# Kernel tuning notes

Measured on AMD Instinct MI355X. Metric: run time of the kernel, lower is better.

Reference implementation:

```python
import jax, jax.numpy as jnp
import numpy as np

N_NODES = 100000
N_EDGES = 1600000
NFEAT = 128
NHID = 128
NCLASS = 40


def gcn_conv(x, W, b, src, dst, n_nodes):
    """PyG-style GCNConv: x' = D^{-1/2}(A+I)D^{-1/2} (x W) + b."""
    h = x @ W  # [N, out]
    loop = jnp.arange(n_nodes, dtype=src.dtype)
    s = jnp.concatenate([src, loop])  # add self-loops
    d = jnp.concatenate([dst, loop])
    deg = jax.ops.segment_sum(jnp.ones_like(s, dtype=h.dtype), d, num_segments=n_nodes)
    dinv = jnp.where(deg > 0, jax.lax.rsqrt(deg), 0.0)
    norm = dinv[s] * dinv[d]  # [E+N]
    msg = h[s] * norm[:, None]  # gather + scale
    out = jax.ops.segment_sum(msg, d, num_segments=n_nodes)  # scatter-add
    return out + b


def setup_inputs() -> dict:
    key = jax.random.key(0)
    ks = jax.random.split(key, 6)
    x = jax.random.normal(ks[0], (N_NODES, NFEAT), dtype=jnp.float32)
    edge_index = jax.random.randint(ks[1], (2, N_EDGES), 0, N_NODES, dtype=jnp.int64)
    sc1 = 1.0 / np.sqrt(NFEAT)
    sc2 = 1.0 / np.sqrt(NHID)
    W1 = jax.random.normal(ks[2], (NFEAT, NHID), dtype=jnp.float32) * sc1
    b1 = jnp.zeros((NHID,), dtype=jnp.float32)
    Wm = jax.random.normal(ks[3], (NHID, NHID), dtype=jnp.float32) * sc2
    bm = jnp.zeros((NHID,), dtype=jnp.float32)
    W2 = jax.random.normal(ks[4], (NHID, NCLASS), dtype=jnp.float32) * sc2
    b2 = jnp.zeros((NCLASS,), dtype=jnp.float32)
    return {"x": x, "edge_index": edge_index, "W1": W1, "b1": b1,
            "Wm": Wm, "bm": bm, "W2": W2, "b2": b2}


def reference(x, edge_index, W1, b1, Wm, bm, W2, b2):
    # StandGCNX forward, eval mode (dropout = identity)
    src, dst = edge_index[0], edge_index[1]
    n = x.shape[0]
    h = jax.nn.relu(gcn_conv(x, W1, b1, src, dst, n))
    h = jax.nn.relu(gcn_conv(h, Wm, bm, src, dst, n))
    out = gcn_conv(h, W2, b2, src, dst, n)
    return out
```

## Files before the change

kernel.cpp:

```cpp
#include <hip/hip_runtime.h>
#include <hip/hip_bf16.h>

typedef __attribute__((ext_vector_type(8))) short bf16x8;
typedef __attribute__((ext_vector_type(4))) float f32x4;

__device__ __forceinline__ ushort bf16rne(float f) {
    uint u = __float_as_uint(f);
    return (ushort)((u + 0x7fffu + ((u >> 16) & 1u)) >> 16);
}
__device__ __forceinline__ void unpack2(uint p, float& a, float& b) {
    a = __uint_as_float(p << 16);
    b = __uint_as_float(p & 0xffff0000u);
}


__global__ __launch_bounds__(256) void k_pre1(const float* __restrict__ W1,
                                              const float* __restrict__ Wm,
                                              const float* __restrict__ W2,
                                              ushort* __restrict__ w1t,
                                              ushort* __restrict__ wmt,
                                              ushort* __restrict__ w2t,
                                              const int* __restrict__ dst,
                                              int* __restrict__ bcnt, int E) {
    __shared__ int hist[512];
    int b = blockIdx.x;
    int t = threadIdx.x;
    if (b < 152) {
        if (b < 64) {
            int i = b * 256 + t; int k = i >> 7, n = i & 127;
            w1t[n * 128 + k] = bf16rne(W1[k * 128 + n]);
        } else if (b < 128) {
            int i = (b - 64) * 256 + t; int k = i >> 7, n = i & 127;
            wmt[n * 128 + k] = bf16rne(Wm[k * 128 + n]);
        } else {
            int i = (b - 128) * 256 + t;
            if (i < 6144) {
                int n = i >> 7, k = i & 127;
                w2t[n * 128 + k] = (n < 40) ? bf16rne(W2[k * 40 + n]) : (ushort)0;
            }
        }
        return;
    }
    hist[t] = 0; hist[t + 256] = 0;
    __syncthreads();
    int off = (b - 152) * 4096;
    int cnt = min(4096, E - off);
    for (int i = t; i < cnt; i += 256) atomicAdd(&hist[dst[off + i] >> 8], 1);
    __syncthreads();
    if (hist[t]) atomicAdd(&bcnt[t], hist[t]);
    if (hist[t + 256]) atomicAdd(&bcnt[t + 256], hist[t + 256]);
}

__global__ void k_bscan(const int* __restrict__ bcnt, int* __restrict__ bbase,
                        int* __restrict__ bcur, int nbuck) {
    __shared__ int s[512];
    int t = threadIdx.x;
    s[t] = (t < nbuck) ? bcnt[t] : 0;
    __syncthreads();
    for (int d = 1; d < 512; d <<= 1) {
        int u = (t >= d) ? s[t - d] : 0;
        __syncthreads();
        if (t >= d) s[t] += u;
        __syncthreads();
    }
    int excl = (t == 0) ? 0 : s[t - 1];
    bbase[t] = excl;
    if (t < nbuck) bcur[t] = excl;
    if (t == 511) bbase[512] = s[511];
}


__global__ __launch_bounds__(256) void k_pack_gemm(const int* __restrict__ src,
                                                   const int* __restrict__ dst,
                                                   int* __restrict__ bcur,
                                                   uint* __restrict__ pairbuf,
                                                   int E, int nbuck, int ntile,
                                                   const float* __restrict__ A,
                                                   const ushort* __restrict__ Wt,
                                                   ushort* __restrict__ C, int M) {
    __shared__ int hist[512];
    __shared__ int scn[512];
    __shared__ int cur[512];
    __shared__ int gbase[512];
    __shared__ uint sorted[4096];
    int t = threadIdx.x;
    if ((int)blockIdx.x >= ntile) {
        int blk = blockIdx.x - ntile;
        int wave = t >> 6, lane = t & 63;
        int m16 = lane & 15, quad = lane >> 4;
        int rowA = blk * 64 + wave * 16 + m16;
        int rA = min(rowA, M - 1);
        const float4* A4 = (const float4*)A;

        f32x4 acc[8];
#pragma unroll
        for (int i = 0; i < 8; i++) acc[i] = (f32x4){0.f, 0.f, 0.f, 0.f};
#pragma unroll
        for (int it = 0; it < 4; it++) {
            float4 f0 = A4[(size_t)rA * 32 + 8 * it + 2 * quad];
            float4 f1 = A4[(size_t)rA * 32 + 8 * it + 2 * quad + 1];
            bf16x8 af;
            af[0] = (short)bf16rne(f0.x); af[1] = (short)bf16rne(f0.y);
            af[2] = (short)bf16rne(f0.z); af[3] = (short)bf16rne(f0.w);
            af[4] = (short)bf16rne(f1.x); af[5] = (short)bf16rne(f1.y);
            af[6] = (short)bf16rne(f1.z); af[7] = (short)bf16rne(f1.w);
#pragma unroll
            for (int nt = 0; nt < 8; nt++) {
                bf16x8 bfr = *(const bf16x8*)(Wt + (size_t)(nt * 16 + m16) * 128 + it * 32 + quad * 8);
                acc[nt] = __builtin_amdgcn_mfma_f32_16x16x32_bf16(af, bfr, acc[nt], 0, 0, 0);
            }
        }
        int rowBase = blk * 64 + wave * 16 + quad * 4;
#pragma unroll
        for (int nt = 0; nt < 8; nt++) {
            int col = nt * 16 + m16;
#pragma unroll
            for (int r = 0; r < 4; r++) {
                int row = rowBase + r;
                if (row < M) C[(size_t)row * 128 + col] = bf16rne(acc[nt][r]);
            }
        }
        return;
    }
    int off = blockIdx.x * 4096;
    int cnt = min(4096, E - off);
    hist[t] = 0; hist[t + 256] = 0;
    __syncthreads();
    for (int i = t; i < cnt; i += 256) {
        int b = dst[off + i] >> 8;
        atomicAdd(&hist[b], 1);
    }
    __syncthreads();
    scn[t] = hist[t]; scn[t + 256] = hist[t + 256];
    __syncthreads();
    for (int d = 1; d < 256; d <<= 1) {
        int u0 = (t >= d) ? scn[t - d] : 0;
        int u1 = (t >= d) ? scn[256 + t - d] : 0;
        __syncthreads();
        if (t >= d) { scn[t] += u0; scn[256 + t] += u1; }
        __syncthreads();
    }
    int tot0 = scn[255];
    scn[256 + t] += tot0;
    __syncthreads();
    cur[t] = (t == 0) ? 0 : scn[t - 1];
    cur[t + 256] = scn[t + 255];
    if (t < nbuck && hist[t] > 0) gbase[t] = atomicAdd(&bcur[t], hist[t]);
    int t2 = t + 256;
    if (t2 < nbuck && hist[t2] > 0) gbase[t2] = atomicAdd(&bcur[t2], hist[t2]);
    __syncthreads();
    for (int i = t; i < cnt; i += 256) {
        int d = dst[off + i];
        int s = src[off + i];
        int b = d >> 8;
        int pos = atomicAdd(&cur[b], 1);
        sorted[pos] = ((uint)(d & 255) << 24) | (uint)s;
    }
    __syncthreads();
    int wid = t >> 6, lane = t & 63;
    for (int b = wid; b < nbuck; b += 4) {
        int n = hist[b];
        if (n == 0) continue;
        int ls = (b == 0) ? 0 : scn[b - 1];
        int gb = gbase[b];
        for (int j = lane; j < n; j += 64)
            pairbuf[gb + j] = sorted[ls + j];
    }
}

#define CSR_CAP 5632
__global__ __launch_bounds__(256) void k_csrbuild(const uint* __restrict__ pairbuf,
                                                  const int* __restrict__ bbase,
                                                  int* __restrict__ rowptr,
                                                  float* __restrict__ dinv,
                                                  int* __restrict__ csr,
                                                  int N, int nbuck) {
    __shared__ int lhist[256];
    __shared__ int scn[256];
    __shared__ int lcur[256];
    __shared__ int lcsr[CSR_CAP];
    int b = blockIdx.x;
    int base = b << 8;
    int nn = min(256, N - base);
    int lo = bbase[b], hi = bbase[b + 1];
    int cnt = hi - lo;
    int t = threadIdx.x;
    lhist[t] = 0;
    __syncthreads();
    for (int i = t; i < cnt; i += 256) atomicAdd(&lhist[pairbuf[lo + i] >> 24], 1);
    __syncthreads();
    int mydeg = lhist[t];
    scn[t] = mydeg;
    __syncthreads();
    for (int d = 1; d < 256; d <<= 1) {
        int u = (t >= d) ? scn[t - d] : 0;
        __syncthreads();
        if (t >= d) scn[t] += u;
        __syncthreads();
    }
    int excl = (t == 0) ? 0 : scn[t - 1];
    lcur[t] = excl;
    if (t < nn) {
        rowptr[base + t] = lo + excl;
        dinv[base + t] = rsqrtf((float)(mydeg + 1));
    }
    if (b == nbuck - 1 && t == 0) rowptr[N] = hi;
    __syncthreads();
    if (cnt <= CSR_CAP) {
        for (int i = t; i < cnt; i += 256) {
            uint p = pairbuf[lo + i];
            int pos = atomicAdd(&lcur[p >> 24], 1);
            lcsr[pos] = (int)(p & 0xFFFFFFu);
        }
        __syncthreads();
        for (int i = t; i < cnt; i += 256) csr[lo + i] = lcsr[i];
    } else {
        for (int i = t; i < cnt; i += 256) {
            uint p = pairbuf[lo + i];
            int pos = lo + atomicAdd(&lcur[p >> 24], 1);
            csr[pos] = (int)(p & 0xFFFFFFu);
        }
    }
}


template <bool EDGE_W>
__device__ __forceinline__ void batch8(const uint* __restrict__ g32, int lane,
                                       int creg, int wreg, int j, int lim,
                                       float& x0, float& x1) {
    uint P[8]; float W[8];
#pragma unroll
    for (int k = 0; k < 8; k++) {
        int idx = j + k;
        int cl = idx < 63 ? idx : 63;
        int s = __builtin_amdgcn_readlane(creg, cl);
        float w = EDGE_W ? __int_as_float(__builtin_amdgcn_readlane(wreg, cl)) : 1.0f;
        W[k] = (idx < lim) ? w : 0.0f;
        P[k] = g32[(size_t)s * 64 + lane];
    }
#pragma unroll
    for (int k = 0; k < 8; k++) {
        float u, v; unpack2(P[k], u, v);
        x0 += u * W[k]; x1 += v * W[k];
    }
}

template <bool EDGE_W>
__device__ __forceinline__ void batch8x2(const uint* __restrict__ g32, int lane,
                                         int cA, int wA, int jA, int limA,
                                         float& a0, float& a1,
                                         int cB, int wB, int jB, int limB,
                                         float& b0, float& b1) {
    uint PA[8], PB[8]; float WA[8], WB[8];
#pragma unroll
    for (int k = 0; k < 8; k++) {
        int idx = jA + k;
        int cl = idx < 63 ? idx : 63;
        int s = __builtin_amdgcn_readlane(cA, cl);
        float w = EDGE_W ? __int_as_float(__builtin_amdgcn_readlane(wA, cl)) : 1.0f;
        WA[k] = (idx < limA) ? w : 0.0f;
        PA[k] = g32[(size_t)s * 64 + lane];
    }
#pragma unroll
    for (int k = 0; k < 8; k++) {
        int idx = jB + k;
        int cl = idx < 63 ? idx : 63;
        int s = __builtin_amdgcn_readlane(cB, cl);
        float w = EDGE_W ? __int_as_float(__builtin_amdgcn_readlane(wB, cl)) : 1.0f;
        WB[k] = (idx < limB) ? w : 0.0f;
        PB[k] = g32[(size_t)s * 64 + lane];
    }
#pragma unroll
    for (int k = 0; k < 8; k++) {
        float u, v; unpack2(PA[k], u, v);
        a0 += u * WA[k]; a1 += v * WA[k];
    }
#pragma unroll
    for (int k = 0; k < 8; k++) {
        float u, v; unpack2(PB[k], u, v);
        b0 += u * WB[k]; b1 += v * WB[k];
    }
}

template <bool EDGE_W>
__device__ __forceinline__ void agg_node_chunked(const uint* __restrict__ g32,
                                                 const int* __restrict__ csr,
                                                 const float* __restrict__ dinv,
                                                 int lane, int e0, int e1,
                                                 float& x0, float& x1) {
    for (int base = e0; base < e1; base += 64) {
        int nc = e1 - base; if (nc > 64) nc = 64;
        int sidx = 0, swi = 0;
        if (lane < nc) {
            sidx = csr[base + lane];
            if (EDGE_W) swi = __float_as_int(dinv[sidx]);
        }
        int nc8 = (nc + 7) & ~7;
        for (int j = 0; j < nc8; j += 8)
            batch8<EDGE_W>(g32, lane, sidx, swi, j, nc, x0, x1);
    }
}

template <int NT, bool EDGE_W>
__device__ __forceinline__ void fused_agg_gemm(const ushort* __restrict__ g,
                                               const float* __restrict__ dinv,
                                               const int* __restrict__ rowptr,
                                               const int* __restrict__ csr,
                                               const float* __restrict__ bias,
                                               const ushort* __restrict__ Wt,
                                               ushort* __restrict__ C,
                                               int M, int ccols) {
    __shared__ ushort hs[32][136];
    int t = threadIdx.x;
    int lane = t & 63;
    int wave = t >> 6;
    const uint* g32 = (const uint*)g;
    float2 bb = ((const float2*)bias)[lane];

    int nodeBase = blockIdx.x * 32 + wave * 8;
    int nd_l = min(nodeBase + lane, M - 1);

    uint srow[8];
#pragma unroll
    for (int i = 0; i < 8; i++) {
        int nd = __builtin_amdgcn_readlane(nd_l, i);
        srow[i] = g32[(size_t)nd * 64 + lane];
    }
    int e0_l = 0, e1_l = 0; float dn_l = 0.f;
    if (lane < 8) {
        e0_l = rowptr[nd_l];
        e1_l = rowptr[nd_l + 1];
        dn_l = dinv[nd_l];
    }
    int c0 = 0, c1 = 0, c2 = 0, c3 = 0;
    int w0 = 0, w1 = 0, w2 = 0, w3 = 0;
    int sp0, sp1, sp2, sp3, Ls0, Ls1, Ls2, Ls3;
    sp0 = __builtin_amdgcn_readlane(e0_l, 0);
    Ls0 = __builtin_amdgcn_readlane(e1_l, 1) - sp0;
    sp1 = __builtin_amdgcn_readlane(e0_l, 2);
    Ls1 = __builtin_amdgcn_readlane(e1_l, 3) - sp1;
    sp2 = __builtin_amdgcn_readlane(e0_l, 4);
    Ls2 = __builtin_amdgcn_readlane(e1_l, 5) - sp2;
    sp3 = __builtin_amdgcn_readlane(e0_l, 6);
    Ls3 = __builtin_amdgcn_readlane(e1_l, 7) - sp3;
    if (Ls0 <= 64 && lane < Ls0) c0 = csr[sp0 + lane];
    if (Ls1 <= 64 && lane < Ls1) c1 = csr[sp1 + lane];
    if (Ls2 <= 64 && lane < Ls2) c2 = csr[sp2 + lane];
    if (Ls3 <= 64 && lane < Ls3) c3 = csr[sp3 + lane];
    if (EDGE_W) {
        if (Ls0 <= 64 && lane < Ls0) w0 = __float_as_int(dinv[c0]);
        if (Ls1 <= 64 && lane < Ls1) w1 = __float_as_int(dinv[c1]);
        if (Ls2 <= 64 && lane < Ls2) w2 = __float_as_int(dinv[c2]);
        if (Ls3 <= 64 && lane < Ls3) w3 = __float_as_int(dinv[c3]);
    }
    int cp[4] = {c0, c1, c2, c3};
    int wp[4] = {w0, w1, w2, w3};
    int spp[4] = {sp0, sp1, sp2, sp3};
    int Lsp[4] = {Ls0, Ls1, Ls2, Ls3};

#pragma unroll
    for (int p = 0; p < 4; p++) {
        int iA = 2 * p, iB = 2 * p + 1;
        int eA0 = __builtin_amdgcn_readlane(e0_l, iA);
        int eA1 = __builtin_amdgcn_readlane(e1_l, iA);
        int eB0 = __builtin_amdgcn_readlane(e0_l, iB);
        int eB1 = __builtin_amdgcn_readlane(e1_l, iB);
        float dnA = __int_as_float(__builtin_amdgcn_readlane(__float_as_int(dn_l), iA));
        float dnB = __int_as_float(__builtin_amdgcn_readlane(__float_as_int(dn_l), iB));
        float a0, a1, b0, b1;
        {
            float u, v;
            unpack2(srow[2 * p], u, v);
            if (EDGE_W) { a0 = u * dnA; a1 = v * dnA; } else { a0 = u; a1 = v; }
            unpack2(srow[2 * p + 1], u, v);
            if (EDGE_W) { b0 = u * dnB; b1 = v * dnB; } else { b0 = u; b1 = v; }
        }
        if (Lsp[p] <= 64) {
            int offA = eA0 - spp[p];
            int offB = eB0 - spp[p];
            int nA = eA1 - eA0, nB = eB1 - eB0;
            int limA = offA + nA, limB = offB + nB;
            int jA = offA, jB = offB;
            int jAend = offA + ((nA + 7) & ~7);
            int jBend = offB + ((nB + 7) & ~7);
            while (jA < jAend && jB < jBend) {
                batch8x2<EDGE_W>(g32, lane, cp[p], wp[p], jA, limA, a0, a1,
                                 cp[p], wp[p], jB, limB, b0, b1);
                jA += 8; jB += 8;
            }
            while (jA < jAend) { batch8<EDGE_W>(g32, lane, cp[p], wp[p], jA, limA, a0, a1); jA += 8; }
            while (jB < jBend) { batch8<EDGE_W>(g32, lane, cp[p], wp[p], jB, limB, b0, b1); jB += 8; }
        } else {
            agg_node_chunked<EDGE_W>(g32, csr, dinv, lane, eA0, eA1, a0, a1);
            agg_node_chunked<EDGE_W>(g32, csr, dinv, lane, eB0, eB1, b0, b1);
        }
        float o0 = fmaxf(a0 * dnA + bb.x, 0.f);
        float o1 = fmaxf(a1 * dnA + bb.y, 0.f);
        float o2 = fmaxf(b0 * dnB + bb.x, 0.f);
        float o3 = fmaxf(b1 * dnB + bb.y, 0.f);
        uint qA = (uint)bf16rne(o0) | ((uint)bf16rne(o1) << 16);
        uint qB = (uint)bf16rne(o2) | ((uint)bf16rne(o3) << 16);
        *(uint*)&hs[wave * 8 + 2 * p][lane * 2] = qA;
        *(uint*)&hs[wave * 8 + 2 * p + 1][lane * 2] = qB;
    }
    __syncthreads();

    int wv = t >> 6, lane6 = t & 63;
    int m16 = lane6 & 15, quad = lane6 >> 4;
    int rowHalf = wv & 1;
    int ntHalf = wv >> 1;
    constexpr int NTH = (NT + 1) / 2;
    int ntStart = ntHalf * NTH;
    int ntEnd = ntHalf ? NT : NTH;

    f32x4 acc[NTH];
#pragma unroll
    for (int i = 0; i < NTH; i++) acc[i] = (f32x4){0.f, 0.f, 0.f, 0.f};
#pragma unroll
    for (int it = 0; it < 4; it++) {
        bf16x8 af = *(const bf16x8*)&hs[rowHalf * 16 + m16][it * 32 + quad * 8];
        for (int nt = ntStart; nt < ntEnd; nt++) {
            bf16x8 bfr = *(const bf16x8*)(Wt + (size_t)(nt * 16 + m16) * 128 + it * 32 + quad * 8);
            acc[nt - ntStart] = __builtin_amdgcn_mfma_f32_16x16x32_bf16(af, bfr, acc[nt - ntStart], 0, 0, 0);
        }
    }
    int rowBase = blockIdx.x * 32 + rowHalf * 16 + quad * 4;
    float dnv[4];
#pragma unroll
    for (int r = 0; r < 4; r++) dnv[r] = dinv[min(rowBase + r, M - 1)];
    for (int nt = ntStart; nt < ntEnd; nt++) {
        int col = nt * 16 + m16;
        if (col >= ccols) continue;
#pragma unroll
        for (int r = 0; r < 4; r++) {
            int row = rowBase + r;
            if (row < M) C[(size_t)row * ccols + col] = bf16rne(acc[nt - ntStart][r] * dnv[r]);
        }
    }
}

__global__ __launch_bounds__(256) void k_fusedA(const ushort* __restrict__ g,
                                                const float* __restrict__ dinv,
                                                const int* __restrict__ rowptr,
                                                const int* __restrict__ csr,
                                                const float* __restrict__ bias,
                                                const ushort* __restrict__ Wt,
                                                ushort* __restrict__ C, int M) {
    fused_agg_gemm<8, true>(g, dinv, rowptr, csr, bias, Wt, C, M, 128);
}

__global__ __launch_bounds__(256) void k_fusedB(const ushort* __restrict__ g,
                                                const float* __restrict__ dinv,
                                                const int* __restrict__ rowptr,
                                                const int* __restrict__ csr,
                                                const float* __restrict__ bias,
                                                const ushort* __restrict__ Wt,
                                                ushort* __restrict__ C, int M) {
    fused_agg_gemm<3, false>(g, dinv, rowptr, csr, bias, Wt, C, M, 40);
}


__global__ __launch_bounds__(256) void k_agg40_b(const ushort* __restrict__ g3,
                                                 const float* __restrict__ dinv,
                                                 const int* __restrict__ rowptr,
                                                 const int* __restrict__ csr,
                                                 const float* __restrict__ bias,
                                                 float* __restrict__ out, int N) {
    int t = threadIdx.x;
    if (t >= 250) return;
    int grp = t / 10;
    int l = t - grp * 10;
    int node = blockIdx.x * 25 + grp;
    if (node >= N) return;
    const uint2* gp = (const uint2*)g3;
    float dn = dinv[node];
    float a0, a1, a2, a3;
    {
        uint2 p = gp[(size_t)node * 10 + l];
        unpack2(p.x, a0, a1);
        unpack2(p.y, a2, a3);
    }
    int e0 = rowptr[node], e1 = rowptr[node + 1];
    int e = e0;
    for (; e + 4 <= e1; e += 4) {
        int s0 = csr[e], s1 = csr[e + 1], s2 = csr[e + 2], s3 = csr[e + 3];
        uint2 p0 = gp[(size_t)s0 * 10 + l];
        uint2 p1 = gp[(size_t)s1 * 10 + l];
        uint2 p2 = gp[(size_t)s2 * 10 + l];
        uint2 p3 = gp[(size_t)s3 * 10 + l];
        float u, v;
        unpack2(p0.x, u, v); a0 += u; a1 += v;
        unpack2(p0.y, u, v); a2 += u; a3 += v;
        unpack2(p1.x, u, v); a0 += u; a1 += v;
        unpack2(p1.y, u, v); a2 += u; a3 += v;
        unpack2(p2.x, u, v); a0 += u; a1 += v;
        unpack2(p2.y, u, v); a2 += u; a3 += v;
        unpack2(p3.x, u, v); a0 += u; a1 += v;
        unpack2(p3.y, u, v); a2 += u; a3 += v;
    }
    for (; e < e1; e++) {
        int s = csr[e];
        uint2 p = gp[(size_t)s * 10 + l];
        float u, v;
        unpack2(p.x, u, v); a0 += u; a1 += v;
        unpack2(p.y, u, v); a2 += u; a3 += v;
    }
    float4 bb = ((const float4*)bias)[l];
    float4 o;
    o.x = a0 * dn + bb.x;
    o.y = a1 * dn + bb.y;
    o.z = a2 * dn + bb.z;
    o.w = a3 * dn + bb.w;
    ((float4*)out)[(size_t)node * 10 + l] = o;
}


extern "C" void kernel_launch(void* const* d_in, const int* in_sizes, int n_in,
                              void* d_out, int out_size, void* d_ws, size_t ws_size,
                              hipStream_t stream) {
    const float* x  = (const float*)d_in[0];
    const int* eidx = (const int*)d_in[1];
    const float* W1 = (const float*)d_in[2];
    const float* b1 = (const float*)d_in[3];
    const float* Wm = (const float*)d_in[4];
    const float* bm = (const float*)d_in[5];
    const float* W2 = (const float*)d_in[6];
    const float* b2 = (const float*)d_in[7];
    float* out = (float*)d_out;

    int N = in_sizes[0] / 128;
    int E = in_sizes[1] / 2;
    const int* src = eidx;
    const int* dst = eidx + E;
    int nbuck = (N + 255) >> 8;
    int ntile = (E + 4095) / 4096;

    char* ws = (char*)d_ws;
    size_t off = 0;
    auto alloc = [&](size_t bytes) -> void* {
        void* p = ws + off;
        off += (bytes + 255) & ~(size_t)255;
        return p;
    };
    float*  dinv    = (float*)alloc((size_t)N * 4);
    int*    rowptr  = (int*)alloc(((size_t)N + 1) * 4);
    int*    csr     = (int*)alloc((size_t)E * 4);
    uint*   pairbuf = (uint*)alloc((size_t)E * 4);
    int*    bcnt    = (int*)alloc(512 * 4);
    int*    bbase   = (int*)alloc(513 * 4);
    int*    bcur    = (int*)alloc(512 * 4);
    ushort* w1t     = (ushort*)alloc(128 * 128 * 2);
    ushort* wmt     = (ushort*)alloc(128 * 128 * 2);
    ushort* w2t     = (ushort*)alloc(48 * 128 * 2);
    ushort* gbuf    = (ushort*)alloc((size_t)N * 128 * 2);
    ushort* gbuf2   = (ushort*)alloc((size_t)N * 128 * 2);
    ushort* g3      = (ushort*)alloc((size_t)N * 40 * 2);

    int gblk64 = (N + 63) / 64;
    int gblk32 = (N + 31) / 32;

    hipMemsetAsync(bcnt, 0, 512 * 4, stream);
    k_pre1<<<152 + ntile, 256, 0, stream>>>(W1, Wm, W2, w1t, wmt, w2t, dst, bcnt, E);
    k_bscan<<<1, 512, 0, stream>>>(bcnt, bbase, bcur, nbuck);
    k_pack_gemm<<<ntile + gblk64, 256, 0, stream>>>(src, dst, bcur, pairbuf, E, nbuck,
                                                    ntile, x, w1t, gbuf, N);
    k_csrbuild<<<nbuck, 256, 0, stream>>>(pairbuf, bbase, rowptr, dinv, csr, N, nbuck);
    k_fusedA<<<gblk32, 256, 0, stream>>>(gbuf, dinv, rowptr, csr, b1, wmt, gbuf2, N);
    k_fusedB<<<gblk32, 256, 0, stream>>>(gbuf2, dinv, rowptr, csr, bm, w2t, g3, N);
    k_agg40_b<<<(N + 24) / 25, 256, 0, stream>>>(g3, dinv, rowptr, csr, b2, out, N);
}
```

Measured before the change: 359.5 us.

## Pad layer-3 features to 64 columns and use wave-cooperative CSR gather

Pads the final projection from 40 to 64 columns so each row of g3 is 128 bytes, which aligns rows for the gather. The last aggregation kernel is rewritten so each half-wave handles one node: it loads up to 32 neighbor indices cooperatively, broadcasts them with readlane, and issues 8 independent loads per step. This targets the serialized per-thread csr reads and the misaligned 80-byte rows. In exchange it reads and writes more g3 bytes, does more GEMM columns in fusedB, and spends padded work when the two nodes sharing a wave have different degrees.

```diff
diff --git a/kernel.cpp b/kernel.cpp
--- a/kernel.cpp
+++ b/kernel.cpp
@@ -25,7 +25,7 @@
     __shared__ int hist[512];
     int b = blockIdx.x;
     int t = threadIdx.x;
-    if (b < 152) {
+    if (b < 160) {
         if (b < 64) {
             int i = b * 256 + t; int k = i >> 7, n = i & 127;
             w1t[n * 128 + k] = bf16rne(W1[k * 128 + n]);
@@ -34,16 +34,14 @@
             wmt[n * 128 + k] = bf16rne(Wm[k * 128 + n]);
         } else {
             int i = (b - 128) * 256 + t;
-            if (i < 6144) {
-                int n = i >> 7, k = i & 127;
-                w2t[n * 128 + k] = (n < 40) ? bf16rne(W2[k * 40 + n]) : (ushort)0;
-            }
+            int n = i >> 7, k = i & 127;
+            w2t[n * 128 + k] = (n < 40) ? bf16rne(W2[k * 40 + n]) : (ushort)0;
         }
         return;
     }
     hist[t] = 0; hist[t + 256] = 0;
     __syncthreads();
-    int off = (b - 152) * 4096;
+    int off = (b - 160) * 4096;
     int cnt = min(4096, E - off);
     for (int i = t; i < cnt; i += 256) atomicAdd(&hist[dst[off + i] >> 8], 1);
     __syncthreads();
@@ -456,7 +454,7 @@
                                                 const float* __restrict__ bias,
                                                 const ushort* __restrict__ Wt,
                                                 ushort* __restrict__ C, int M) {
-    fused_agg_gemm<3, false>(g, dinv, rowptr, csr, bias, Wt, C, M, 40);
+    fused_agg_gemm<4, false>(g, dinv, rowptr, csr, bias, Wt, C, M, 64);
 }
 
 
@@ -467,51 +465,64 @@
                                                  const float* __restrict__ bias,
                                                  float* __restrict__ out, int N) {
     int t = threadIdx.x;
-    if (t >= 250) return;
-    int grp = t / 10;
-    int l = t - grp * 10;
-    int node = blockIdx.x * 25 + grp;
-    if (node >= N) return;
-    const uint2* gp = (const uint2*)g3;
-    float dn = dinv[node];
-    float a0, a1, a2, a3;
+    int wave = t >> 6, lane = t & 63;
+    int half = lane >> 5, hl = lane & 31;
+    const uint* gp = (const uint*)g3;
+
+    int node0 = (blockIdx.x * 4 + wave) * 2;
+    int nA = min(node0, N - 1);
+    int nB = min(node0 + 1, N - 1);
+    int myNode = half ? nB : nA;
+    float dn = dinv[myNode];
+    int e0A = rowptr[nA], e1A = rowptr[nA + 1];
+    int e0B = rowptr[nB], e1B = rowptr[nB + 1];
+
+    float a0, a1;
     {
-        uint2 p = gp[(size_t)node * 10 + l];
-        unpack2(p.x, a0, a1);
-        unpack2(p.y, a2, a3);
-    }
-    int e0 = rowptr[node], e1 = rowptr[node + 1];
-    int e = e0;
-    for (; e + 4 <= e1; e += 4) {
-        int s0 = csr[e], s1 = csr[e + 1], s2 = csr[e + 2], s3 = csr[e + 3];
-        uint2 p0 = gp[(size_t)s0 * 10 + l];
-        uint2 p1 = gp[(size_t)s1 * 10 + l];
-        uint2 p2 = gp[(size_t)s2 * 10 + l];
-        uint2 p3 = gp[(size_t)s3 * 10 + l];
-        float u, v;
-        unpack2(p0.x, u, v); a0 += u; a1 += v;
-        unpack2(p0.y, u, v); a2 += u; a3 += v;
-        unpack2(p1.x, u, v); a0 += u; a1 += v;
-        unpack2(p1.y, u, v); a2 += u; a3 += v;
-        unpack2(p2.x, u, v); a0 += u; a1 += v;
-        unpack2(p2.y, u, v); a2 += u; a3 += v;
-        unpack2(p3.x, u, v); a0 += u; a1 += v;
-        unpack2(p3.y, u, v); a2 += u; a3 += v;
-    }
-    for (; e < e1; e++) {
-        int s = csr[e];
-        uint2 p = gp[(size_t)s * 10 + l];
-        float u, v;
-        unpack2(p.x, u, v); a0 += u; a1 += v;
-        unpack2(p.y, u, v); a2 += u; a3 += v;
-    }
-    float4 bb = ((const float4*)bias)[l];
-    float4 o;
-    o.x = a0 * dn + bb.x;
-    o.y = a1 * dn + bb.y;
-    o.z = a2 * dn + bb.z;
-    o.w = a3 * dn + bb.w;
-    ((float4*)out)[(size_t)node * 10 + l] = o;
+        uint p = gp[(size_t)myNode * 32 + hl];
+        unpack2(p, a0, a1);
+    }
+    int baseA = e0A, baseB = e0B;
+    while (baseA < e1A || baseB < e1B) {
+        int ncA = e1A - baseA; if (ncA > 32) ncA = 32; if (ncA < 0) ncA = 0;
+        int ncB = e1B - baseB; if (ncB > 32) ncB = 32; if (ncB < 0) ncB = 0;
+        int myBase = half ? baseB : baseA;
+        int myNc = half ? ncB : ncA;
+        int sidx = 0;
+        if (hl < myNc) sidx = csr[myBase + hl];
+        int lim = myNc;
+        int m8A = (ncA + 7) & ~7;
+        int m8B = (ncB + 7) & ~7;
+        int m8 = m8A > m8B ? m8A : m8B;
+        for (int j = 0; j < m8; j += 8) {
+            uint P[8]; float W[8];
+#pragma unroll
+            for (int k = 0; k < 8; k++) {
+                int idx = j + k;
+                int cl = idx < 31 ? idx : 31;
+                int sA = __builtin_amdgcn_readlane(sidx, cl);
+                int sB = __builtin_amdgcn_readlane(sidx, 32 + cl);
+                int s = half ? sB : sA;
+                W[k] = (idx < lim) ? 1.0f : 0.0f;
+                P[k] = gp[(size_t)s * 32 + hl];
+            }
+#pragma unroll
+            for (int k = 0; k < 8; k++) {
+                float u, v; unpack2(P[k], u, v);
+                a0 += u * W[k]; a1 += v * W[k];
+            }
+        }
+        baseA += ncA;
+        baseB += ncB;
+    }
+    int onode = node0 + half;
+    if (onode < N && hl < 20) {
+        float2 bb = ((const float2*)bias)[hl];
+        float2 o;
+        o.x = a0 * dn + bb.x;
+        o.y = a1 * dn + bb.y;
+        ((float2*)out)[(size_t)onode * 20 + hl] = o;
+    }
 }
 
 
@@ -551,21 +562,21 @@
     int*    bcur    = (int*)alloc(512 * 4);
     ushort* w1t     = (ushort*)alloc(128 * 128 * 2);
     ushort* wmt     = (ushort*)alloc(128 * 128 * 2);
-    ushort* w2t     = (ushort*)alloc(48 * 128 * 2);
+    ushort* w2t     = (ushort*)alloc(64 * 128 * 2);
     ushort* gbuf    = (ushort*)alloc((size_t)N * 128 * 2);
     ushort* gbuf2   = (ushort*)alloc((size_t)N * 128 * 2);
-    ushort* g3      = (ushort*)alloc((size_t)N * 40 * 2);
+    ushort* g3      = (ushort*)alloc((size_t)N * 64 * 2);
 
     int gblk64 = (N + 63) / 64;
     int gblk32 = (N + 31) / 32;
 
     hipMemsetAsync(bcnt, 0, 512 * 4, stream);
-    k_pre1<<<152 + ntile, 256, 0, stream>>>(W1, Wm, W2, w1t, wmt, w2t, dst, bcnt, E);
+    k_pre1<<<160 + ntile, 256, 0, stream>>>(W1, Wm, W2, w1t, wmt, w2t, dst, bcnt, E);
     k_bscan<<<1, 512, 0, stream>>>(bcnt, bbase, bcur, nbuck);
     k_pack_gemm<<<ntile + gblk64, 256, 0, stream>>>(src, dst, bcur, pairbuf, E, nbuck,
                                                     ntile, x, w1t, gbuf, N);
     k_csrbuild<<<nbuck, 256, 0, stream>>>(pairbuf, bbase, rowptr, dinv, csr, N, nbuck);
     k_fusedA<<<gblk32, 256, 0, stream>>>(gbuf, dinv, rowptr, csr, b1, wmt, gbuf2, N);
     k_fusedB<<<gblk32, 256, 0, stream>>>(gbuf2, dinv, rowptr, csr, bm, w2t, g3, N);
-    k_agg40_b<<<(N + 24) / 25, 256, 0, stream>>>(g3, dinv, rowptr, csr, b2, out, N);
-}
+    k_agg40_b<<<(N + 7) / 8, 256, 0, stream>>>(g3, dinv, rowptr, csr, b2, out, N);
+}
```

Measured after the change: 365.1 us. About the same (+1.5%).
